# Optimization experiments

Hardware: AMD Instinct MI355X
Metric: run time of the kernel (lower is better)

The kernel has to match this reference:

```python
import jax, jax.numpy as jnp
import numpy as np
from jax import lax

POOL = 7          # pool_size
SR = 2            # bilinear sampling ratio per bin axis
SCALE = 0.125     # spatial_scale for FPN level p3 (1/8)
NUM_CLASSES = 21
SCORE_T = 0.05
NMS_T = 0.5
MAXDET = 100
LBL_OFF = 1.0e4   # per-class box offset for batched NMS


def setup_inputs() -> dict:
    key = jax.random.key(0)
    ks = jax.random.split(key, 8)
    feature_map = jax.random.normal(ks[0], (256, 100, 100), jnp.float32)
    # proposals: valid xyxy boxes inside an 800x800 image
    xy = jax.random.uniform(ks[1], (1000, 2), jnp.float32, 0.0, 700.0)
    wh = jax.random.uniform(ks[2], (1000, 2), jnp.float32, 16.0, 128.0)
    proposals = jnp.concatenate([xy, xy + wh], axis=1)
    fin = 256 * POOL * POOL
    w1 = jax.random.normal(ks[3], (fin, 1024), jnp.float32) * np.sqrt(2.0 / 1024)
    w2 = jax.random.normal(ks[4], (1024, 1024), jnp.float32) * np.sqrt(2.0 / 1024)
    wc = jax.random.normal(ks[5], (1024, NUM_CLASSES), jnp.float32) * 0.01
    wb = jax.random.normal(ks[6], (1024, NUM_CLASSES * 4), jnp.float32) * 0.001
    return {
        'feature_map': feature_map, 'proposals': proposals,
        'w1': w1, 'b1': jnp.zeros((1024,), jnp.float32),
        'w2': w2, 'b2': jnp.zeros((1024,), jnp.float32),
        'wc': wc, 'bc': jnp.zeros((NUM_CLASSES,), jnp.float32),
        'wb': wb, 'bb': jnp.zeros((NUM_CLASSES * 4,), jnp.float32),
    }


def _roi_align(fm, rois):
    """torchvision roi_align, aligned=True, sampling_ratio=SR. fm:[C,H,W] rois:[N,4] xyxy."""
    C, H, W = fm.shape
    b = rois * SCALE - 0.5  # aligned=True half-pixel shift
    x1, y1 = b[:, 0], b[:, 1]
    bw = (b[:, 2] - b[:, 0]) / POOL
    bh = (b[:, 3] - b[:, 1]) / POOL
    # sample offsets within a roi, in units of bin width: [POOL*SR]
    off = (jnp.arange(POOL, dtype=jnp.float32)[:, None]
           + (jnp.arange(SR, dtype=jnp.float32)[None, :] + 0.5) / SR).reshape(-1)
    X = x1[:, None] + off[None, :] * bw[:, None]  # [N, PS]
    Y = y1[:, None] + off[None, :] * bh[:, None]  # [N, PS]

    def axis_prep(v, size):
        valid = (v >= -1.0) & (v <= size)
        v = jnp.clip(v, 0.0, size - 1.0)
        v0 = jnp.floor(v)
        i0 = v0.astype(jnp.int32)
        i1 = jnp.minimum(i0 + 1, size - 1)
        whi = v - v0
        return i0, i1, 1.0 - whi, whi, valid

    x0, x1i, wx0, wx1, vx = axis_prep(X, W)
    y0, y1i, wy0, wy1, vy = axis_prep(Y, H)

    def gath(yi, xi):
        # outer-product advanced indexing -> [C, N, PS, PS]
        return fm[:, yi[:, :, None], xi[:, None, :]]

    val = ((wy0[:, :, None] * wx0[:, None, :]) * gath(y0, x0)
           + (wy0[:, :, None] * wx1[:, None, :]) * gath(y0, x1i)
           + (wy1[:, :, None] * wx0[:, None, :]) * gath(y1i, x0)
           + (wy1[:, :, None] * wx1[:, None, :]) * gath(y1i, x1i))
    val = val * (vy[:, :, None] & vx[:, None, :]).astype(val.dtype)
    N = rois.shape[0]
    val = val.reshape(C, N, POOL, SR, POOL, SR).mean(axis=(3, 5))  # avg over samples
    return val.transpose(1, 0, 2, 3)  # [N, C, POOL, POOL]


def _decode(deltas, boxes):
    """deltas:[N,K,4], boxes:[N,4] xyxy -> [N,K,4] xyxy."""
    w = boxes[:, 2] - boxes[:, 0]
    h = boxes[:, 3] - boxes[:, 1]
    cx = boxes[:, 0] + 0.5 * w
    cy = boxes[:, 1] + 0.5 * h
    dx, dy, dw, dh = deltas[..., 0], deltas[..., 1], deltas[..., 2], deltas[..., 3]
    pcx = dx * w[:, None] + cx[:, None]
    pcy = dy * h[:, None] + cy[:, None]
    pw = jnp.exp(dw) * w[:, None]
    ph = jnp.exp(dh) * h[:, None]
    return jnp.stack([pcx - 0.5 * pw, pcy - 0.5 * ph,
                      pcx + 0.5 * pw, pcy + 0.5 * ph], axis=-1)


def _iou_one(b, B):
    ix1 = jnp.maximum(b[0], B[:, 0]); iy1 = jnp.maximum(b[1], B[:, 1])
    ix2 = jnp.minimum(b[2], B[:, 2]); iy2 = jnp.minimum(b[3], B[:, 3])
    inter = jnp.clip(ix2 - ix1, 0.0) * jnp.clip(iy2 - iy1, 0.0)
    a = (b[2] - b[0]) * (b[3] - b[1])
    A = (B[:, 2] - B[:, 0]) * (B[:, 3] - B[:, 1])
    return inter / (a + A - inter + 1e-9)


def _forward(feature_map, proposals, w1, b1, w2, b2, wc, bc, wb, bb):
    N = proposals.shape[0]
    pooled = _roi_align(feature_map, proposals).reshape(N, -1)  # [N, 12544]
    x = jax.nn.relu(pooled @ w1 + b1)
    x = jax.nn.relu(x @ w2 + b2)
    cls_logits = x @ wc + bc                 # [N, 21]
    box_deltas = x @ wb + bb                 # [N, 84]
    scores = jax.nn.softmax(cls_logits, axis=1)
    fg_scores = scores[:, 1:]                              # [N, 20] drop background
    fg_deltas = box_deltas.reshape(N, NUM_CLASSES, 4)[:, 1:, :]
    boxes = _decode(fg_deltas, proposals)                  # [N, 20, 4]
    K = NUM_CLASSES - 1
    boxes_f = boxes.reshape(N * K, 4)
    scores_f = fg_scores.reshape(N * K)
    labels_f = jnp.tile(jnp.arange(1, NUM_CLASSES, dtype=jnp.int32), N)
    # score threshold as masking (fixed shapes)
    cand = jnp.where(scores_f > SCORE_T, scores_f, -1.0)
    boxes_off = boxes_f + labels_f.astype(boxes_f.dtype)[:, None] * LBL_OFF

    def step(sw, _):
        i = jnp.argmax(sw)
        s = sw[i]
        iou = _iou_one(boxes_off[i], boxes_off)
        sw = jnp.where(iou > NMS_T, -jnp.inf, sw)  # self-IoU=1 removes i too
        return sw, (i, s)

    _, (keep_idx, keep_sc) = lax.scan(step, cand, None, length=MAXDET)
    valid = keep_sc > SCORE_T
    out_boxes = boxes_f[keep_idx] * valid[:, None].astype(boxes_f.dtype)
    out_scores = jnp.where(valid, keep_sc, 0.0)
    out_labels = jnp.where(valid, labels_f[keep_idx], 0)
    return out_boxes, out_scores, out_labels


def reference(feature_map, proposals, w1, b1, w2, b2, wc, bc, wb, bb):
    return _forward(feature_map, proposals, w1, b1, w2, b2, wc, bc, wb, bb)
```

## Files before the change

### kernel.cpp

```cpp
#include <hip/hip_runtime.h>
#include <math.h>

#define NPROP 1000
#define CCH 256
#define FH 100
#define FW 100
#define POOLSZ 7
#define FEAT 12544
#define HID 1024
#define NCLS 21
#define NHEAD 105
#define NCAND 20000
#define SCORE_T 0.05f
#define NMS_T 0.5f
#define MAXDET 100

typedef _Float16 f16;
typedef __attribute__((ext_vector_type(8))) _Float16 f16x8;
typedef __attribute__((ext_vector_type(4))) float f32x4;

__global__ __launch_bounds__(256) void k_transpose(const float* __restrict__ fm,
                                                   float* __restrict__ fmT) {
    __shared__ float lds[64 * 257];
    int posbase = blockIdx.x * 64;
    int tid = threadIdx.x;
    int cq = tid >> 6;
    int pl = tid & 63;
    int pos = posbase + pl;
    bool pok = pos < FH * FW;
    for (int c0 = 0; c0 < CCH; c0 += 4) {
        int c = c0 + cq;
        float v = pok ? fm[c * (FH * FW) + pos] : 0.f;
        lds[pl * 257 + c] = v;
    }
    __syncthreads();
    for (int p = 0; p < 64; ++p) {
        int pos2 = posbase + p;
        if (pos2 < FH * FW) fmT[(size_t)pos2 * CCH + tid] = lds[p * 257 + tid];
    }
}

__global__ __launch_bounds__(256) void k_roi(const float* __restrict__ fmT,
                                             const float* __restrict__ rois,
                                             float* __restrict__ pooled) {
    int n = blockIdx.x;
    int tid = threadIdx.x;
    __shared__ float wx0[14], wx1[14], wy0[14], wy1[14];
    __shared__ int ix0[14], ix1[14], iy0[14], iy1[14], vx[14], vy[14];
    __shared__ float outb[FEAT];

    if (tid < 28) {
        int axis = tid / 14;
        int j = tid % 14;
        float p0 = rois[n * 4 + axis];
        float p1 = rois[n * 4 + 2 + axis];
        float b0 = p0 * 0.125f - 0.5f;
        float b1 = p1 * 0.125f - 0.5f;
        float bsz = (b1 - b0) / 7.0f;
        int p = j >> 1, s = j & 1;
        float off = (float)p + ((float)s + 0.5f) / 2.0f;
        float v = b0 + off * bsz;
        float size = 100.0f;
        int valid = (v >= -1.0f && v <= size) ? 1 : 0;
        v = fminf(fmaxf(v, 0.0f), size - 1.0f);
        float v0 = floorf(v);
        int i0 = (int)v0;
        int i1 = min(i0 + 1, 99);
        float w1v = v - v0;
        float w0v = 1.0f - w1v;
        if (axis == 0) { ix0[j] = i0 * CCH; ix1[j] = i1 * CCH; wx0[j] = w0v; wx1[j] = w1v; vx[j] = valid; }
        else           { iy0[j] = i0 * (FW * CCH); iy1[j] = i1 * (FW * CCH); wy0[j] = w0v; wy1[j] = w1v; vy[j] = valid; }
    }
    __syncthreads();

    int c = tid;
    for (int py = 0; py < POOLSZ; ++py) {
        for (int px = 0; px < POOLSZ; ++px) {
            float acc = 0.f;
            #pragma unroll
            for (int sy = 0; sy < 2; ++sy) {
                int jy = py * 2 + sy;
                if (!vy[jy]) continue;
                float fy0 = wy0[jy], fy1 = wy1[jy];
                int y0 = iy0[jy], y1 = iy1[jy];
                #pragma unroll
                for (int sx = 0; sx < 2; ++sx) {
                    int jx = px * 2 + sx;
                    if (!vx[jx]) continue;
                    float fx0 = wx0[jx], fx1 = wx1[jx];
                    int x0 = ix0[jx], x1 = ix1[jx];
                    float a00 = fmT[y0 + x0 + c];
                    float a01 = fmT[y0 + x1 + c];
                    float a10 = fmT[y1 + x0 + c];
                    float a11 = fmT[y1 + x1 + c];
                    acc += fy0 * (fx0 * a00 + fx1 * a01) + fy1 * (fx0 * a10 + fx1 * a11);
                }
            }
            outb[c * 49 + py * 7 + px] = acc * 0.25f;
        }
    }
    __syncthreads();
    size_t base = (size_t)n * FEAT;
    for (int o = tid; o < FEAT; o += 256)
        pooled[base + o] = outb[o];
}

__global__ __launch_bounds__(256) void k_gemm_mfma(const float* __restrict__ A,
                                                   const float* __restrict__ B,
                                                   float* __restrict__ P,
                                                   int M, int K, int nt) {
    __shared__ f16 Ah[2][2048], Al[2][2048], Bh[2][2048], Bl[2][2048];
    int tid = threadIdx.x;
    int n0 = blockIdx.x * 64;
    int m0 = blockIdx.y * 64;
    int kz = blockIdx.z;
    int kbase0 = kz * nt * 32;

    int a_row = tid >> 2;
    int a_kq  = tid & 3;
    int b_n   = tid & 63;
    int b_kg  = tid >> 6;

    int wave = tid >> 6, lane = tid & 63;
    int wr = (wave >> 1) * 32, wc = (wave & 1) * 32;
    int lhi = lane >> 4, llo = lane & 15;

    f32x4 accm[2][2] = {};
    f32x4 accc[2][2] = {};

    float aS[8], bS[8];
    const float* Arow = A + (size_t)(m0 + a_row) * K;
    bool arow_ok = (m0 + a_row) < M;

    int a_st = a_kq * 512 + ((a_row ^ a_kq) << 3);
    int b_st = b_kg * 512 + (b_n << 3);
    int a_rd0 = lhi * 512 + (((wr + 0  + llo) ^ lhi) << 3);
    int a_rd1 = lhi * 512 + (((wr + 16 + llo) ^ lhi) << 3);
    int b_rd0 = lhi * 512 + ((wc + 0  + llo) << 3);
    int b_rd1 = lhi * 512 + ((wc + 16 + llo) << 3);

    auto LOAD = [&](int t) {
        int kb = kbase0 + t * 32;
        if (arow_ok) {
            const float* ap = Arow + kb + a_kq * 8;
            float4 v0 = *(const float4*)(ap);
            float4 v1 = *(const float4*)(ap + 4);
            aS[0] = v0.x; aS[1] = v0.y; aS[2] = v0.z; aS[3] = v0.w;
            aS[4] = v1.x; aS[5] = v1.y; aS[6] = v1.z; aS[7] = v1.w;
        } else {
            #pragma unroll
            for (int j = 0; j < 8; ++j) aS[j] = 0.f;
        }
        const float* bp = B + (size_t)(kb + b_kg * 8) * 1024 + n0 + b_n;
        #pragma unroll
        for (int j = 0; j < 8; ++j) bS[j] = bp[(size_t)j * 1024];
    };
    auto STORE = [&](int buf) {
        f16x8 vh, vl;
        #pragma unroll
        for (int j = 0; j < 8; ++j) {
            f16 h = (f16)aS[j];
            vh[j] = h;
            vl[j] = (f16)((aS[j] - (float)h) * 4096.0f);
        }
        *(f16x8*)&Ah[buf][a_st] = vh;
        *(f16x8*)&Al[buf][a_st] = vl;
        #pragma unroll
        for (int j = 0; j < 8; ++j) {
            f16 h = (f16)bS[j];
            vh[j] = h;
            vl[j] = (f16)((bS[j] - (float)h) * 4096.0f);
        }
        *(f16x8*)&Bh[buf][b_st] = vh;
        *(f16x8*)&Bl[buf][b_st] = vl;
    };

    LOAD(0);
    STORE(0);
    __syncthreads();

    for (int t = 0; t < nt; ++t) {
        int cur = t & 1;
        if (t + 1 < nt) LOAD(t + 1);
        {
            f16x8 ah0 = *(f16x8*)&Ah[cur][a_rd0];
            f16x8 ah1 = *(f16x8*)&Ah[cur][a_rd1];
            f16x8 bh0 = *(f16x8*)&Bh[cur][b_rd0];
            f16x8 bh1 = *(f16x8*)&Bh[cur][b_rd1];
            f16x8 al0 = *(f16x8*)&Al[cur][a_rd0];
            f16x8 al1 = *(f16x8*)&Al[cur][a_rd1];
            f16x8 bl0 = *(f16x8*)&Bl[cur][b_rd0];
            f16x8 bl1 = *(f16x8*)&Bl[cur][b_rd1];
            accm[0][0] = __builtin_amdgcn_mfma_f32_16x16x32_f16(ah0, bh0, accm[0][0], 0, 0, 0);
            accm[0][1] = __builtin_amdgcn_mfma_f32_16x16x32_f16(ah0, bh1, accm[0][1], 0, 0, 0);
            accm[1][0] = __builtin_amdgcn_mfma_f32_16x16x32_f16(ah1, bh0, accm[1][0], 0, 0, 0);
            accm[1][1] = __builtin_amdgcn_mfma_f32_16x16x32_f16(ah1, bh1, accm[1][1], 0, 0, 0);
            accc[0][0] = __builtin_amdgcn_mfma_f32_16x16x32_f16(ah0, bl0, accc[0][0], 0, 0, 0);
            accc[0][1] = __builtin_amdgcn_mfma_f32_16x16x32_f16(ah0, bl1, accc[0][1], 0, 0, 0);
            accc[1][0] = __builtin_amdgcn_mfma_f32_16x16x32_f16(ah1, bl0, accc[1][0], 0, 0, 0);
            accc[1][1] = __builtin_amdgcn_mfma_f32_16x16x32_f16(ah1, bl1, accc[1][1], 0, 0, 0);
            accc[0][0] = __builtin_amdgcn_mfma_f32_16x16x32_f16(al0, bh0, accc[0][0], 0, 0, 0);
            accc[0][1] = __builtin_amdgcn_mfma_f32_16x16x32_f16(al0, bh1, accc[0][1], 0, 0, 0);
            accc[1][0] = __builtin_amdgcn_mfma_f32_16x16x32_f16(al1, bh0, accc[1][0], 0, 0, 0);
            accc[1][1] = __builtin_amdgcn_mfma_f32_16x16x32_f16(al1, bh1, accc[1][1], 0, 0, 0);
        }
        if (t + 1 < nt) {
            STORE(cur ^ 1);
            __syncthreads();
        }
    }

    const float inv = 1.0f / 4096.0f;
    #pragma unroll
    for (int mi = 0; mi < 2; ++mi) {
        #pragma unroll
        for (int r = 0; r < 4; ++r) {
            int row = m0 + wr + mi * 16 + lhi * 4 + r;
            if (row < M) {
                #pragma unroll
                for (int ni = 0; ni < 2; ++ni) {
                    int col = n0 + wc + ni * 16 + llo;
                    float v = accm[mi][ni][r] + accc[mi][ni][r] * inv;
                    P[(size_t)kz * 1048576 + (size_t)row * 1024 + col] = v;
                }
            }
        }
    }
}

__global__ __launch_bounds__(256) void k_fuse(const float* __restrict__ P,
                                              const float* __restrict__ bias,
                                              float* __restrict__ out) {
    int t = blockIdx.x * 256 + threadIdx.x;
    float4 p0 = ((const float4*)P)[t];
    float4 p1 = ((const float4*)(P + 1048576))[t];
    float4 b  = ((const float4*)bias)[t & 255];
    float4 v;
    v.x = fmaxf(p0.x + p1.x + b.x, 0.f);
    v.y = fmaxf(p0.y + p1.y + b.y, 0.f);
    v.z = fmaxf(p0.z + p1.z + b.z, 0.f);
    v.w = fmaxf(p0.w + p1.w + b.w, 0.f);
    ((float4*)out)[t] = v;
}

__global__ __launch_bounds__(128) void k_heads(const float* __restrict__ x2,
                                               const float* __restrict__ wc,
                                               const float* __restrict__ bc,
                                               const float* __restrict__ wb,
                                               const float* __restrict__ bb,
                                               float* __restrict__ logits) {
    int r0 = blockIdx.x * 4;
    __shared__ float xs[4][HID];
    for (int i = threadIdx.x; i < 4 * HID; i += 128) {
        int rr = i >> 10, kk = i & 1023;
        xs[rr][kk] = x2[(size_t)(r0 + rr) * HID + kk];
    }
    __syncthreads();
    int j = threadIdx.x;
    if (j < NHEAD) {
        float a0 = 0.f, a1 = 0.f, a2 = 0.f, a3 = 0.f;
        if (j < NCLS) {
            for (int k = 0; k < HID; ++k) {
                float w = wc[k * NCLS + j];
                a0 = fmaf(xs[0][k], w, a0);
                a1 = fmaf(xs[1][k], w, a1);
                a2 = fmaf(xs[2][k], w, a2);
                a3 = fmaf(xs[3][k], w, a3);
            }
            float b = bc[j];
            a0 += b; a1 += b; a2 += b; a3 += b;
        } else {
            int jb = j - NCLS;
            for (int k = 0; k < HID; ++k) {
                float w = wb[k * 84 + jb];
                a0 = fmaf(xs[0][k], w, a0);
                a1 = fmaf(xs[1][k], w, a1);
                a2 = fmaf(xs[2][k], w, a2);
                a3 = fmaf(xs[3][k], w, a3);
            }
            float b = bb[jb];
            a0 += b; a1 += b; a2 += b; a3 += b;
        }
        logits[(size_t)(r0 + 0) * NHEAD + j] = a0;
        logits[(size_t)(r0 + 1) * NHEAD + j] = a1;
        logits[(size_t)(r0 + 2) * NHEAD + j] = a2;
        logits[(size_t)(r0 + 3) * NHEAD + j] = a3;
    }
}

__global__ __launch_bounds__(256) void k_prep(const float* __restrict__ logits,
                                              const float* __restrict__ rois,
                                              float* __restrict__ boxes,
                                              float* __restrict__ cand,
                                              float* __restrict__ boxesT) {
    int n = blockIdx.x * 256 + threadIdx.x;
    if (n >= NPROP) return;
    const float* L = logits + (size_t)n * NHEAD;
    float m = L[0];
    #pragma unroll
    for (int k = 1; k < NCLS; ++k) m = fmaxf(m, L[k]);
    float sum = 0.f;
    #pragma unroll
    for (int k = 0; k < NCLS; ++k) sum += expf(L[k] - m);

    float p0 = rois[n * 4 + 0], p1 = rois[n * 4 + 1];
    float p2 = rois[n * 4 + 2], p3 = rois[n * 4 + 3];
    float w = p2 - p0, h = p3 - p1;
    float cx = p0 + 0.5f * w, cy = p1 + 0.5f * h;

    for (int k = 1; k < NCLS; ++k) {
        int i = n * 20 + (k - 1);
        float s = expf(L[k] - m) / sum;
        const float* D = L + NCLS + k * 4;
        float dx = D[0], dy = D[1], dw = D[2], dh = D[3];
        float pcx = dx * w + cx;
        float pcy = dy * h + cy;
        float pw = expf(dw) * w;
        float ph = expf(dh) * h;
        float b0 = pcx - 0.5f * pw;
        float b1 = pcy - 0.5f * ph;
        float b2 = pcx + 0.5f * pw;
        float b3 = pcy + 0.5f * ph;
        boxes[(size_t)i * 4 + 0] = b0;
        boxes[(size_t)i * 4 + 1] = b1;
        boxes[(size_t)i * 4 + 2] = b2;
        boxes[(size_t)i * 4 + 3] = b3;
        cand[i] = (s > SCORE_T) ? s : -__builtin_inff();
        float offv = (float)k * 10000.0f;
        ((float4*)boxesT)[(k - 1) * 1024 + n] =
            make_float4(b0 + offv, b1 + offv, b2 + offv, b3 + offv);
    }
}

__global__ __launch_bounds__(1024) void k_nms(const float* __restrict__ cand,
                                              const float* __restrict__ boxes,
                                              const float* __restrict__ boxesT,
                                              float* __restrict__ out) {
    __shared__ float s_lds[20 * 1024];
    __shared__ unsigned long long gkeys[2];
    __shared__ unsigned long long wkeys[MAXDET];
    __shared__ float sb[4];
    int tid = threadIdx.x;
    if (tid < 2) gkeys[tid] = 0ULL;
    if (tid < MAXDET) wkeys[tid] = 0ULL;

    unsigned long long tkey = 0ULL;
    if (tid < NPROP) {
        #pragma unroll
        for (int i = 0; i < 20; ++i) {
            float v = cand[tid * 20 + i];
            s_lds[i * 1024 + tid] = v;
            if (v > 0.0f) {
                unsigned long long k =
                    ((unsigned long long)__float_as_uint(v) << 32) |
                    (unsigned long long)(0xFFFFFFFFu - (unsigned)(tid * 20 + i));
                if (k > tkey) tkey = k;
            }
        }
    } else {
        #pragma unroll
        for (int i = 0; i < 20; ++i) s_lds[i * 1024 + tid] = -__builtin_inff();
    }
    __syncthreads();

    for (int it = 0; it < MAXDET; ++it) {
        int cur = it & 1;
        unsigned long long k = tkey;
        #pragma unroll
        for (int off = 32; off > 0; off >>= 1) {
            unsigned long long o = __shfl_down(k, off);
            if (o > k) k = o;
        }
        if ((tid & 63) == 0) atomicMax(&gkeys[cur], k);
        __syncthreads();
        unsigned long long g = gkeys[cur];
        int bi = (int)(0xFFFFFFFFu - (unsigned)(g & 0xFFFFFFFFu));
        int own = bi / 20;
        int wcls = bi - own * 20;
        if (tid == 0) {
            gkeys[cur ^ 1] = 0ULL;
            wkeys[it] = g;
        }
        if (g != 0ULL && own == tid) {
            float4 b = ((const float4*)boxesT)[wcls * 1024 + tid];
            sb[0] = b.x; sb[1] = b.y; sb[2] = b.z; sb[3] = b.w;
        }
        __syncthreads();
        if (g == 0ULL) break;

        float sv = s_lds[wcls * 1024 + tid];
        bool killed = false;
        if (sv > 0.0f) {
            float4 c = ((const float4*)boxesT)[wcls * 1024 + tid];
            float q0 = sb[0], q1 = sb[1], q2 = sb[2], q3 = sb[3];
            float qa = (q2 - q0) * (q3 - q1);
            float ix1 = fmaxf(q0, c.x), iy1 = fmaxf(q1, c.y);
            float ix2 = fminf(q2, c.z), iy2 = fminf(q3, c.w);
            float inter = fmaxf(ix2 - ix1, 0.f) * fmaxf(iy2 - iy1, 0.f);
            float A2 = (c.z - c.x) * (c.w - c.y);
            float iou = inter / (qa + A2 - inter + 1e-9f);
            if (iou > NMS_T) {
                s_lds[wcls * 1024 + tid] = -__builtin_inff();
                killed = true;
            }
        }
        if (killed) {
            tkey = 0ULL;
            #pragma unroll
            for (int i = 0; i < 20; ++i) {
                float v = s_lds[i * 1024 + tid];
                if (v > 0.0f) {
                    unsigned long long kk =
                        ((unsigned long long)__float_as_uint(v) << 32) |
                        (unsigned long long)(0xFFFFFFFFu - (unsigned)(tid * 20 + i));
                    if (kk > tkey) tkey = kk;
                }
            }
        }
    }

    __syncthreads();
    if (tid < MAXDET) {
        unsigned long long g = wkeys[tid];
        if (g != 0ULL) {
            int bi = (int)(0xFFFFFFFFu - (unsigned)(g & 0xFFFFFFFFu));
            float4 b = ((const float4*)boxes)[bi];
            out[tid * 4 + 0] = b.x; out[tid * 4 + 1] = b.y;
            out[tid * 4 + 2] = b.z; out[tid * 4 + 3] = b.w;
            out[400 + tid] = __uint_as_float((unsigned)(g >> 32));
            out[500 + tid] = (float)(bi - (bi / 20) * 20 + 1);
        } else {
            out[tid * 4 + 0] = 0.f; out[tid * 4 + 1] = 0.f;
            out[tid * 4 + 2] = 0.f; out[tid * 4 + 3] = 0.f;
            out[400 + tid] = 0.f;
            out[500 + tid] = 0.f;
        }
    }
}

extern "C" void kernel_launch(void* const* d_in, const int* in_sizes, int n_in,
                              void* d_out, int out_size, void* d_ws, size_t ws_size,
                              hipStream_t stream) {
    const float* fm   = (const float*)d_in[0];
    const float* rois = (const float*)d_in[1];
    const float* w1   = (const float*)d_in[2];
    const float* b1   = (const float*)d_in[3];
    const float* w2   = (const float*)d_in[4];
    const float* b2   = (const float*)d_in[5];
    const float* wc   = (const float*)d_in[6];
    const float* bc   = (const float*)d_in[7];
    const float* wb   = (const float*)d_in[8];
    const float* bb   = (const float*)d_in[9];
    float* out = (float*)d_out;

    float* ws = (float*)d_ws;
    float* fmT    = ws;
    float* P      = ws;
    float* pooled = fmT + 2560000;
    float* x1     = pooled + 12544000;
    float* x2     = x1 + 1024000;
    float* logits = x2 + 1024000;
    float* boxes  = logits + 105000;
    float* cand   = boxes + 80000;
    float* boxesT = pooled;

    k_transpose<<<157, 256, 0, stream>>>(fm, fmT);
    k_roi<<<NPROP, 256, 0, stream>>>(fmT, rois, pooled);
    k_gemm_mfma<<<dim3(16, 16, 2), 256, 0, stream>>>(pooled, w1, P, NPROP, FEAT, 196);
    k_fuse<<<1000, 256, 0, stream>>>(P, b1, x1);
    k_gemm_mfma<<<dim3(16, 16, 2), 256, 0, stream>>>(x1, w2, P, NPROP, HID, 16);
    k_fuse<<<1000, 256, 0, stream>>>(P, b2, x2);
    k_heads<<<250, 128, 0, stream>>>(x2, wc, bc, wb, bb, logits);
    k_prep<<<4, 256, 0, stream>>>(logits, rois, boxes, cand, boxesT);
    k_nms<<<1, 1024, 0, stream>>>(cand, boxes, boxesT, out);
}
```

Measured before the change: 797.3 us.

## Split NMS into per-class blocks with bitmask suppression and a top-k merge

Replaces the single-block greedy NMS, which ran 100 serial argmax+IoU iterations over all 20000 candidates, with one block per class. Each class block sorts its candidates with a bitonic sort, builds a pairwise IoU suppression bitmask in workspace, and resolves greedy keeps in a single wavefront. A small merge kernel then takes the top 100 across the per-class sorted keep lists. This relies on the class offset making cross-class IoU zero. It adds an extra launch, an O(V^2) IoU mask per class, and global-memory mask traffic.

```diff
diff --git a/kernel.cpp b/kernel.cpp
--- a/kernel.cpp
+++ b/kernel.cpp
@@ -332,96 +332,138 @@
     }
 }
 
-__global__ __launch_bounds__(1024) void k_nms(const float* __restrict__ cand,
-                                              const float* __restrict__ boxes,
-                                              const float* __restrict__ boxesT,
-                                              float* __restrict__ out) {
-    __shared__ float s_lds[20 * 1024];
-    __shared__ unsigned long long gkeys[2];
-    __shared__ unsigned long long wkeys[MAXDET];
-    __shared__ float sb[4];
+__global__ __launch_bounds__(256) void k_nms_cls(const float* __restrict__ cand,
+                                                 const float* __restrict__ boxesT,
+                                                 unsigned long long* __restrict__ maskws,
+                                                 unsigned long long* __restrict__ accG,
+                                                 int* __restrict__ accN) {
+    __shared__ unsigned long long skeys[1024];
+    __shared__ float4 bbox[1024];
+    __shared__ unsigned long long accL[MAXDET];
+    __shared__ int sV, sM;
     int tid = threadIdx.x;
-    if (tid < 2) gkeys[tid] = 0ULL;
-    if (tid < MAXDET) wkeys[tid] = 0ULL;
-
-    unsigned long long tkey = 0ULL;
-    if (tid < NPROP) {
-        #pragma unroll
-        for (int i = 0; i < 20; ++i) {
-            float v = cand[tid * 20 + i];
-            s_lds[i * 1024 + tid] = v;
+    int c = blockIdx.x;
+    if (tid == 0) { sV = 0; sM = 0; }
+
+    for (int n = tid; n < 1024; n += 256) {
+        unsigned long long key = 0ULL;
+        if (n < NPROP) {
+            float v = cand[n * 20 + c];
             if (v > 0.0f) {
-                unsigned long long k =
-                    ((unsigned long long)__float_as_uint(v) << 32) |
-                    (unsigned long long)(0xFFFFFFFFu - (unsigned)(tid * 20 + i));
-                if (k > tkey) tkey = k;
-            }
-        }
-    } else {
-        #pragma unroll
-        for (int i = 0; i < 20; ++i) s_lds[i * 1024 + tid] = -__builtin_inff();
-    }
-    __syncthreads();
-
-    for (int it = 0; it < MAXDET; ++it) {
-        int cur = it & 1;
-        unsigned long long k = tkey;
-        #pragma unroll
-        for (int off = 32; off > 0; off >>= 1) {
-            unsigned long long o = __shfl_down(k, off);
-            if (o > k) k = o;
-        }
-        if ((tid & 63) == 0) atomicMax(&gkeys[cur], k);
+                key = ((unsigned long long)__float_as_uint(v) << 32) |
+                      (unsigned long long)(0xFFFFFFFFu - (unsigned)(n * 20 + c));
+            }
+        }
+        skeys[n] = key;
+    }
+    __syncthreads();
+
+    for (int k = 2; k <= 1024; k <<= 1) {
+        for (int j = k >> 1; j > 0; j >>= 1) {
+            for (int t = tid; t < 512; t += 256) {
+                int i = ((t & ~(j - 1)) << 1) | (t & (j - 1));
+                int l = i | j;
+                unsigned long long a = skeys[i], b = skeys[l];
+                bool up = (i & k) == 0;
+                if (up ? (a < b) : (a > b)) { skeys[i] = b; skeys[l] = a; }
+            }
+            __syncthreads();
+        }
+    }
+
+    {
+        int cnt = 0;
+        for (int n = tid; n < 1024; n += 256)
+            if (skeys[n] != 0ULL) ++cnt;
+        if (cnt) atomicAdd(&sV, cnt);
+    }
+    __syncthreads();
+    int V = sV;
+
+    if (V > 0) {
+        for (int r = tid; r < V; r += 256) {
+            unsigned idx = 0xFFFFFFFFu - (unsigned)(skeys[r] & 0xFFFFFFFFu);
+            int n = idx / 20;
+            bbox[r] = ((const float4*)boxesT)[c * 1024 + n];
+        }
         __syncthreads();
-        unsigned long long g = gkeys[cur];
-        int bi = (int)(0xFFFFFFFFu - (unsigned)(g & 0xFFFFFFFFu));
-        int own = bi / 20;
-        int wcls = bi - own * 20;
-        if (tid == 0) {
-            gkeys[cur ^ 1] = 0ULL;
-            wkeys[it] = g;
-        }
-        if (g != 0ULL && own == tid) {
-            float4 b = ((const float4*)boxesT)[wcls * 1024 + tid];
-            sb[0] = b.x; sb[1] = b.y; sb[2] = b.z; sb[3] = b.w;
+
+        int W = (V + 63) >> 6;
+        unsigned long long* mrow = maskws + (size_t)c * 16384;
+        for (int j = tid; j < V; j += 256) {
+            float4 a = bbox[j];
+            float qa = (a.z - a.x) * (a.w - a.y);
+            for (int w = 0; w < W; ++w) {
+                unsigned long long m = 0ULL;
+                if (w >= (j >> 6)) {
+                    #pragma unroll 4
+                    for (int b = 0; b < 64; ++b) {
+                        int kk = w * 64 + b;
+                        if (kk > j && kk < V) {
+                            float4 cb = bbox[kk];
+                            float ix1 = fmaxf(a.x, cb.x), iy1 = fmaxf(a.y, cb.y);
+                            float ix2 = fminf(a.z, cb.z), iy2 = fminf(a.w, cb.w);
+                            float inter = fmaxf(ix2 - ix1, 0.f) * fmaxf(iy2 - iy1, 0.f);
+                            float A2 = (cb.z - cb.x) * (cb.w - cb.y);
+                            float iou = inter / (qa + A2 - inter + 1e-9f);
+                            if (iou > NMS_T) m |= (1ULL << b);
+                        }
+                    }
+                }
+                mrow[j * 16 + w] = m;
+            }
         }
         __syncthreads();
-        if (g == 0ULL) break;
-
-        float sv = s_lds[wcls * 1024 + tid];
-        bool killed = false;
-        if (sv > 0.0f) {
-            float4 c = ((const float4*)boxesT)[wcls * 1024 + tid];
-            float q0 = sb[0], q1 = sb[1], q2 = sb[2], q3 = sb[3];
-            float qa = (q2 - q0) * (q3 - q1);
-            float ix1 = fmaxf(q0, c.x), iy1 = fmaxf(q1, c.y);
-            float ix2 = fminf(q2, c.z), iy2 = fminf(q3, c.w);
-            float inter = fmaxf(ix2 - ix1, 0.f) * fmaxf(iy2 - iy1, 0.f);
-            float A2 = (c.z - c.x) * (c.w - c.y);
-            float iou = inter / (qa + A2 - inter + 1e-9f);
-            if (iou > NMS_T) {
-                s_lds[wcls * 1024 + tid] = -__builtin_inff();
-                killed = true;
-            }
-        }
-        if (killed) {
-            tkey = 0ULL;
+
+        if (tid < 64) {
+            unsigned long long sup = 0ULL;
+            int m = 0;
+            for (int j = 0; j < V && m < MAXDET; ++j) {
+                unsigned long long sw = __shfl(sup, j >> 6);
+                if (!((sw >> (j & 63)) & 1ULL)) {
+                    if (tid == 0) accL[m] = skeys[j];
+                    if (tid < W) sup |= mrow[j * 16 + tid];
+                    ++m;
+                }
+            }
+            if (tid == 0) sM = m;
+        }
+    }
+    __syncthreads();
+    int m = sM;
+    if (tid < m) accG[c * MAXDET + tid] = accL[tid];
+    if (tid == 0) accN[c] = m;
+}
+
+__global__ __launch_bounds__(128) void k_nms_merge(const unsigned long long* __restrict__ accG,
+                                                   const int* __restrict__ accN,
+                                                   const float* __restrict__ boxes,
+                                                   float* __restrict__ out) {
+    __shared__ unsigned long long picks[MAXDET];
+    int tid = threadIdx.x;
+    if (tid < 64) {
+        int c = tid;
+        int cnt = (c < 20) ? accN[c] : 0;
+        int ptr = 0;
+        unsigned long long key = (cnt > 0) ? accG[c * MAXDET] : 0ULL;
+        for (int it = 0; it < MAXDET; ++it) {
+            unsigned long long k = key;
             #pragma unroll
-            for (int i = 0; i < 20; ++i) {
-                float v = s_lds[i * 1024 + tid];
-                if (v > 0.0f) {
-                    unsigned long long kk =
-                        ((unsigned long long)__float_as_uint(v) << 32) |
-                        (unsigned long long)(0xFFFFFFFFu - (unsigned)(tid * 20 + i));
-                    if (kk > tkey) tkey = kk;
-                }
-            }
-        }
-    }
-
+            for (int off = 32; off > 0; off >>= 1) {
+                unsigned long long o = __shfl_down(k, off);
+                if (o > k) k = o;
+            }
+            unsigned long long g = __shfl(k, 0);
+            if (tid == 0) picks[it] = g;
+            if (g != 0ULL && key == g) {
+                ++ptr;
+                key = (ptr < cnt) ? accG[c * MAXDET + ptr] : 0ULL;
+            }
+        }
+    }
     __syncthreads();
     if (tid < MAXDET) {
-        unsigned long long g = wkeys[tid];
+        unsigned long long g = picks[tid];
         if (g != 0ULL) {
             int bi = (int)(0xFFFFFFFFu - (unsigned)(g & 0xFFFFFFFFu));
             float4 b = ((const float4*)boxes)[bi];
@@ -463,6 +505,9 @@
     float* boxes  = logits + 105000;
     float* cand   = boxes + 80000;
     float* boxesT = pooled;
+    unsigned long long* maskws = (unsigned long long*)(pooled + 131072);
+    unsigned long long* accG   = (unsigned long long*)(pooled + 786432);
+    int* accN                  = (int*)(pooled + 790432);
 
     k_transpose<<<157, 256, 0, stream>>>(fm, fmT);
     k_roi<<<NPROP, 256, 0, stream>>>(fmT, rois, pooled);
@@ -472,5 +517,6 @@
     k_fuse<<<1000, 256, 0, stream>>>(P, b2, x2);
     k_heads<<<250, 128, 0, stream>>>(x2, wc, bc, wb, bb, logits);
     k_prep<<<4, 256, 0, stream>>>(logits, rois, boxes, cand, boxesT);
-    k_nms<<<1, 1024, 0, stream>>>(cand, boxes, boxesT, out);
-}
+    k_nms_cls<<<20, 256, 0, stream>>>(cand, boxesT, maskws, accG, accN);
+    k_nms_merge<<<1, 128, 0, stream>>>(accG, accN, boxes, out);
+}
```

After: 980.4 us. 1.23x slower.

## Split NMS into per-class blocks with a final top-100 merge

Applied to the files above, without the earlier changes.

Replaces the single-block greedy NMS over all 20000 candidates with 20 blocks, one per class, each running up to 100 greedy picks over its 1000 boxes held in registers. Because the label offset makes boxes of different classes disjoint, per-class suppression is independent. A small merge kernel then combines the sorted per-class pick lists into the global top 100. The cost being targeted is the serial single-block loop with its LDS rescans. In exchange it adds one kernel launch and workspace buffers placed inside the pooled region.

```diff
diff --git a/kernel.cpp b/kernel.cpp
--- a/kernel.cpp
+++ b/kernel.cpp
@@ -332,40 +332,46 @@
     }
 }
 
-__global__ __launch_bounds__(1024) void k_nms(const float* __restrict__ cand,
-                                              const float* __restrict__ boxes,
-                                              const float* __restrict__ boxesT,
-                                              float* __restrict__ out) {
-    __shared__ float s_lds[20 * 1024];
+__global__ __launch_bounds__(256) void k_nms_cls(const float* __restrict__ cand,
+                                                 const float* __restrict__ boxesT,
+                                                 unsigned long long* __restrict__ accG,
+                                                 int* __restrict__ accN) {
     __shared__ unsigned long long gkeys[2];
-    __shared__ unsigned long long wkeys[MAXDET];
-    __shared__ float sb[4];
+    __shared__ unsigned long long accL[MAXDET];
+    __shared__ float sb4[4];
+    __shared__ int sM;
     int tid = threadIdx.x;
-    if (tid < 2) gkeys[tid] = 0ULL;
-    if (tid < MAXDET) wkeys[tid] = 0ULL;
-
-    unsigned long long tkey = 0ULL;
-    if (tid < NPROP) {
-        #pragma unroll
-        for (int i = 0; i < 20; ++i) {
-            float v = cand[tid * 20 + i];
-            s_lds[i * 1024 + tid] = v;
-            if (v > 0.0f) {
-                unsigned long long k =
-                    ((unsigned long long)__float_as_uint(v) << 32) |
-                    (unsigned long long)(0xFFFFFFFFu - (unsigned)(tid * 20 + i));
-                if (k > tkey) tkey = k;
-            }
-        }
-    } else {
-        #pragma unroll
-        for (int i = 0; i < 20; ++i) s_lds[i * 1024 + tid] = -__builtin_inff();
+    int c = blockIdx.x;
+    if (tid == 0) { gkeys[0] = 0ULL; gkeys[1] = 0ULL; sM = MAXDET; }
+
+    float s[4];
+    float4 bx[4];
+    #pragma unroll
+    for (int r = 0; r < 4; ++r) {
+        int n = tid + (r << 8);
+        if (n < NPROP) {
+            s[r] = cand[n * 20 + c];
+            bx[r] = ((const float4*)boxesT)[c * 1024 + n];
+        } else {
+            s[r] = -__builtin_inff();
+            bx[r] = make_float4(0.f, 0.f, 0.f, 0.f);
+        }
     }
     __syncthreads();
 
     for (int it = 0; it < MAXDET; ++it) {
         int cur = it & 1;
-        unsigned long long k = tkey;
+        unsigned long long k = 0ULL;
+        #pragma unroll
+        for (int r = 0; r < 4; ++r) {
+            if (s[r] > 0.0f) {
+                int n = tid + (r << 8);
+                unsigned long long kk =
+                    ((unsigned long long)__float_as_uint(s[r]) << 32) |
+                    (unsigned long long)(0xFFFFFFFFu - (unsigned)(n * 20 + c));
+                if (kk > k) k = kk;
+            }
+        }
         #pragma unroll
         for (int off = 32; off > 0; off >>= 1) {
             unsigned long long o = __shfl_down(k, off);
@@ -374,54 +380,72 @@
         if ((tid & 63) == 0) atomicMax(&gkeys[cur], k);
         __syncthreads();
         unsigned long long g = gkeys[cur];
-        int bi = (int)(0xFFFFFFFFu - (unsigned)(g & 0xFFFFFFFFu));
-        int own = bi / 20;
-        int wcls = bi - own * 20;
         if (tid == 0) {
             gkeys[cur ^ 1] = 0ULL;
-            wkeys[it] = g;
-        }
-        if (g != 0ULL && own == tid) {
-            float4 b = ((const float4*)boxesT)[wcls * 1024 + tid];
-            sb[0] = b.x; sb[1] = b.y; sb[2] = b.z; sb[3] = b.w;
+            accL[it] = g;
+            if (g == 0ULL) sM = it;
+        }
+        if (g != 0ULL) {
+            int n_win = (int)(0xFFFFFFFFu - (unsigned)(g & 0xFFFFFFFFu)) / 20;
+            if ((n_win & 255) == tid) {
+                float4 b = bx[n_win >> 8];
+                sb4[0] = b.x; sb4[1] = b.y; sb4[2] = b.z; sb4[3] = b.w;
+            }
         }
         __syncthreads();
         if (g == 0ULL) break;
 
-        float sv = s_lds[wcls * 1024 + tid];
-        bool killed = false;
-        if (sv > 0.0f) {
-            float4 c = ((const float4*)boxesT)[wcls * 1024 + tid];
-            float q0 = sb[0], q1 = sb[1], q2 = sb[2], q3 = sb[3];
-            float qa = (q2 - q0) * (q3 - q1);
-            float ix1 = fmaxf(q0, c.x), iy1 = fmaxf(q1, c.y);
-            float ix2 = fminf(q2, c.z), iy2 = fminf(q3, c.w);
-            float inter = fmaxf(ix2 - ix1, 0.f) * fmaxf(iy2 - iy1, 0.f);
-            float A2 = (c.z - c.x) * (c.w - c.y);
-            float iou = inter / (qa + A2 - inter + 1e-9f);
-            if (iou > NMS_T) {
-                s_lds[wcls * 1024 + tid] = -__builtin_inff();
-                killed = true;
-            }
-        }
-        if (killed) {
-            tkey = 0ULL;
+        float q0 = sb4[0], q1 = sb4[1], q2 = sb4[2], q3 = sb4[3];
+        float qa = (q2 - q0) * (q3 - q1);
+        #pragma unroll
+        for (int r = 0; r < 4; ++r) {
+            if (s[r] > 0.0f) {
+                float4 cb = bx[r];
+                float ix1 = fmaxf(q0, cb.x), iy1 = fmaxf(q1, cb.y);
+                float ix2 = fminf(q2, cb.z), iy2 = fminf(q3, cb.w);
+                float inter = fmaxf(ix2 - ix1, 0.f) * fmaxf(iy2 - iy1, 0.f);
+                float A2 = (cb.z - cb.x) * (cb.w - cb.y);
+                float iou = inter / (qa + A2 - inter + 1e-9f);
+                if (iou > NMS_T) s[r] = -__builtin_inff();
+            }
+        }
+    }
+
+    __syncthreads();
+    int mm = sM;
+    if (tid < mm) accG[c * MAXDET + tid] = accL[tid];
+    if (tid == 0) accN[c] = mm;
+}
+
+__global__ __launch_bounds__(128) void k_nms_merge(const unsigned long long* __restrict__ accG,
+                                                   const int* __restrict__ accN,
+                                                   const float* __restrict__ boxes,
+                                                   float* __restrict__ out) {
+    __shared__ unsigned long long picks[MAXDET];
+    int tid = threadIdx.x;
+    if (tid < 64) {
+        int c = tid;
+        int cnt = (c < 20) ? accN[c] : 0;
+        int ptr = 0;
+        unsigned long long key = (cnt > 0) ? accG[c * MAXDET] : 0ULL;
+        for (int it = 0; it < MAXDET; ++it) {
+            unsigned long long k = key;
             #pragma unroll
-            for (int i = 0; i < 20; ++i) {
-                float v = s_lds[i * 1024 + tid];
-                if (v > 0.0f) {
-                    unsigned long long kk =
-                        ((unsigned long long)__float_as_uint(v) << 32) |
-                        (unsigned long long)(0xFFFFFFFFu - (unsigned)(tid * 20 + i));
-                    if (kk > tkey) tkey = kk;
-                }
-            }
-        }
-    }
-
+            for (int off = 32; off > 0; off >>= 1) {
+                unsigned long long o = __shfl_down(k, off);
+                if (o > k) k = o;
+            }
+            unsigned long long g = __shfl(k, 0);
+            if (tid == 0) picks[it] = g;
+            if (g != 0ULL && key == g) {
+                ++ptr;
+                key = (ptr < cnt) ? accG[c * MAXDET + ptr] : 0ULL;
+            }
+        }
+    }
     __syncthreads();
     if (tid < MAXDET) {
-        unsigned long long g = wkeys[tid];
+        unsigned long long g = picks[tid];
         if (g != 0ULL) {
             int bi = (int)(0xFFFFFFFFu - (unsigned)(g & 0xFFFFFFFFu));
             float4 b = ((const float4*)boxes)[bi];
@@ -463,6 +487,8 @@
     float* boxes  = logits + 105000;
     float* cand   = boxes + 80000;
     float* boxesT = pooled;
+    unsigned long long* accG   = (unsigned long long*)(pooled + 131072);
+    int* accN                  = (int*)(pooled + 135072);
 
     k_transpose<<<157, 256, 0, stream>>>(fm, fmT);
     k_roi<<<NPROP, 256, 0, stream>>>(fmT, rois, pooled);
@@ -472,5 +498,6 @@
     k_fuse<<<1000, 256, 0, stream>>>(P, b2, x2);
     k_heads<<<250, 128, 0, stream>>>(x2, wc, bc, wb, bb, logits);
     k_prep<<<4, 256, 0, stream>>>(logits, rois, boxes, cand, boxesT);
-    k_nms<<<1, 1024, 0, stream>>>(cand, boxes, boxesT, out);
-}
+    k_nms_cls<<<20, 256, 0, stream>>>(cand, boxesT, accG, accN);
+    k_nms_merge<<<1, 128, 0, stream>>>(accG, accN, boxes, out);
+}
```

New measurement: 745.5 us. 1.07x faster.
